# Kernel tuning notes

Hardware: AMD Instinct MI355X
Metric: run time of the kernel (lower is better)

The kernel has to match this reference:

```python
import jax, jax.numpy as jnp
import numpy as np

N = 50000      # nodes
E = 800000     # random edges (self-loops added in reference, per PyG GATConv default)
F_IN = 128
B = 512        # graphs in the batch
NEG_SLOPE = 0.2  # PyG GATConv leaky_relu default


def setup_inputs() -> dict:
    key = jax.random.key(0)
    ks = jax.random.split(key, 12)
    def w(k, shape, fan_in):
        return jax.random.normal(k, shape, jnp.float32) / np.sqrt(fan_in)
    return {
        "x": jax.random.normal(ks[0], (N, F_IN), jnp.float32),
        "edge_index": jax.random.randint(ks[1], (2, E), 0, N, dtype=jnp.int32),
        "batch": jnp.sort(jax.random.randint(ks[2], (N,), 0, B, dtype=jnp.int32)),
        "W1": w(ks[3], (F_IN, 4 * 64), F_IN),
        "a_src1": w(ks[4], (4, 64), 64),
        "a_dst1": w(ks[5], (4, 64), 64),
        "b1": jnp.zeros((4 * 64,), jnp.float32),
        "W2": w(ks[6], (256, 1 * 128), 256),
        "a_src2": w(ks[7], (1, 128), 128),
        "a_dst2": w(ks[8], (1, 128), 128),
        "b2": jnp.zeros((128,), jnp.float32),
        "Wl": w(ks[9], (128, 1), 128),
        "bl": jnp.zeros((1,), jnp.float32),
    }


def gat_layer(x, src, dst, W, a_src, a_dst, b, n):
    H, Fo = a_src.shape
    h = (x @ W).reshape(n, H, Fo)                      # [N,H,Fo]
    alpha_s = jnp.einsum("nhf,hf->nh", h, a_src)       # [N,H]
    alpha_d = jnp.einsum("nhf,hf->nh", h, a_dst)
    e = jax.nn.leaky_relu(alpha_s[src] + alpha_d[dst], NEG_SLOPE)  # [E,H]
    # segment softmax over incoming edges of each dst node
    m = jax.ops.segment_max(e, dst, num_segments=n)    # [N,H]; self-loops => every node hit
    ex = jnp.exp(e - m[dst])
    den = jax.ops.segment_sum(ex, dst, num_segments=n)
    alpha = ex / den[dst]                              # [E,H]
    out = jax.ops.segment_sum(h[src] * alpha[:, :, None], dst, num_segments=n)
    return out.reshape(n, H * Fo) + b


def reference(x, edge_index, batch, W1, a_src1, a_dst1, b1, W2, a_src2, a_dst2, b2, Wl, bl):
    n = x.shape[0]
    loops = jnp.arange(n, dtype=edge_index.dtype)
    src = jnp.concatenate([edge_index[0], loops])
    dst = jnp.concatenate([edge_index[1], loops])
    h = jax.nn.elu(gat_layer(x, src, dst, W1, a_src1, a_dst1, b1, n))
    h = jax.nn.elu(gat_layer(h, src, dst, W2, a_src2, a_dst2, b2, n))
    # dropout omitted (inference)
    sums = jax.ops.segment_sum(h, batch, num_segments=B)
    cnt = jax.ops.segment_sum(jnp.ones((n,), h.dtype), batch, num_segments=B)
    g = sums / jnp.maximum(cnt, 1.0)[:, None]          # global_mean_pool -> [B,128]
    return jax.nn.sigmoid(g @ Wl + bl).reshape(-1)     # [B]
```

## Files before the change

kernel.cpp:

```cpp
#include <hip/hip_runtime.h>
#include <hip/hip_bf16.h>

#define NN 50000
#define EE 800000
#define ETOT 850000
#define BB 512
#define CAP 64
#define NPART 8
#define DPP 6250

typedef __hip_bfloat16 bf16;
typedef __attribute__((ext_vector_type(8))) __bf16 v8bf;
typedef __attribute__((ext_vector_type(4))) float f32x4;

__device__ __forceinline__ float lo2f(unsigned int u) {
    return __uint_as_float(u << 16);
}
__device__ __forceinline__ float hi2f(unsigned int u) {
    return __uint_as_float(u & 0xffff0000u);
}
__device__ __forceinline__ float us2f(unsigned short u) {
    return __uint_as_float(((unsigned int)u) << 16);
}
__device__ __forceinline__ unsigned short f2bfbits(float f) {
    bf16 h = __float2bfloat16(f);
    return *reinterpret_cast<unsigned short*>(&h);
}
__device__ __forceinline__ float lrelu_exp(float ev) {
    ev = ev > 0.f ? ev : 0.2f * ev;
    return __expf(fminf(ev, 80.f));
}

__global__ void k_prep(const float* __restrict__ W1, const float* __restrict__ W2,
                       bf16* __restrict__ wt1, bf16* __restrict__ wt2,
                       int* __restrict__ deg) {
    int idx = blockIdx.x * blockDim.x + threadIdx.x;
    if (idx < 256 * 128) {
        int c = idx >> 7, k = idx & 127;
        wt1[idx] = __float2bfloat16(W1[k * 256 + c]);
    } else {
        int j = idx - 256 * 128;
        int c = j >> 8, k = j & 255;
        wt2[j] = __float2bfloat16(W2[k * 128 + c]);
    }
    if (idx < NN) deg[idx] = 0;
}

__global__ void k_scatter(const int* __restrict__ srcArr, const int* __restrict__ dstArr,
                          int* __restrict__ deg, int* __restrict__ csrc) {
    int part = blockIdx.x & (NPART - 1);
    int e = (blockIdx.x >> 3) * 256 + threadIdx.x;
    if (e >= ETOT) return;
    int d, s;
    if (e < EE) { d = dstArr[e]; s = srcArr[e]; }
    else        { d = e - EE;    s = d; }
    d = min(max(d, 0), NN - 1);
    s = min(max(s, 0), NN - 1);
    int lo = part * DPP;
    if (d >= lo && d < lo + DPP) {
        int p = atomicAdd(&deg[d], 1);
        if (p < CAP) csrc[d * CAP + p] = s;
    }
}

__global__ __launch_bounds__(256, 2)
void k_gemm1(const float* __restrict__ x, const bf16* __restrict__ wt1,
             const float* __restrict__ aw_s, const float* __restrict__ aw_d,
             bf16* __restrict__ h1, float* __restrict__ as1,
             float* __restrict__ ad1) {
    int n0 = blockIdx.x * 32;
    int t = threadIdx.x;
    __shared__ bf16 xs[32 * 136];
    for (int i = 0; i < 4; i++) {
        int idx = t + 256 * i;
        int r = idx >> 5, c4 = idx & 31;
        float4 v = make_float4(0.f, 0.f, 0.f, 0.f);
        if (n0 + r < NN) v = *(const float4*)(x + (size_t)(n0 + r) * 128 + c4 * 4);
        ushort4 o;
        o.x = f2bfbits(v.x); o.y = f2bfbits(v.y);
        o.z = f2bfbits(v.z); o.w = f2bfbits(v.w);
        *(ushort4*)(&xs[r * 136 + c4 * 4]) = o;
    }
    __syncthreads();

    int wv = t >> 6, lane = t & 63;
    int q = lane >> 4, r16 = lane & 15;
    int rowBase = (wv & 1) * 16;
    int colBase = (wv >> 1) * 128;

    f32x4 acc[8];
#pragma unroll
    for (int ct = 0; ct < 8; ct++) acc[ct] = (f32x4){0.f, 0.f, 0.f, 0.f};

#pragma unroll
    for (int kt = 0; kt < 4; kt++) {
        v8bf va = *(const v8bf*)(&xs[(rowBase + r16) * 136 + kt * 32 + q * 8]);
#pragma unroll
        for (int ct = 0; ct < 8; ct++) {
            v8bf vb = *(const v8bf*)(wt1 + (size_t)(colBase + ct * 16 + r16) * 128 + kt * 32 + q * 8);
            acc[ct] = __builtin_amdgcn_mfma_f32_16x16x32_bf16(va, vb, acc[ct], 0, 0, 0);
        }
    }

    float wsv[8], wdv[8];
#pragma unroll
    for (int ct = 0; ct < 8; ct++) {
        int col = colBase + ct * 16 + r16;
        wsv[ct] = aw_s[col];
        wdv[ct] = aw_d[col];
    }

    float ps[4][2], pd[4][2];
#pragma unroll
    for (int reg = 0; reg < 4; reg++) {
        ps[reg][0] = 0.f; ps[reg][1] = 0.f;
        pd[reg][0] = 0.f; pd[reg][1] = 0.f;
    }

#pragma unroll
    for (int reg = 0; reg < 4; reg++) {
        int node = n0 + rowBase + q * 4 + reg;
        bool ok = node < NN;
#pragma unroll
        for (int ct = 0; ct < 8; ct++) {
            float v = acc[ct][reg];
            if (ok) h1[(size_t)node * 256 + colBase + ct * 16 + r16] = __float2bfloat16(v);
            ps[reg][ct >> 2] += v * wsv[ct];
            pd[reg][ct >> 2] += v * wdv[ct];
        }
    }

#pragma unroll
    for (int reg = 0; reg < 4; reg++) {
        int node = n0 + rowBase + q * 4 + reg;
        bool ok = node < NN;
#pragma unroll
        for (int lh = 0; lh < 2; lh++) {
            float a = ps[reg][lh], b = pd[reg][lh];
            for (int mask = 1; mask <= 8; mask <<= 1) {
                a += __shfl_xor(a, mask);
                b += __shfl_xor(b, mask);
            }
            if (r16 == 0 && ok) {
                int head = (wv >> 1) * 2 + lh;
                as1[node * 4 + head] = a;
                ad1[node * 4 + head] = b;
            }
        }
    }
}

__global__ __launch_bounds__(128, 8)
void k_gather1(const int* __restrict__ csrc, const int* __restrict__ deg,
               const bf16* __restrict__ h1, const float* __restrict__ as1,
               const float* __restrict__ ad1, const float* __restrict__ b1,
               bf16* __restrict__ x2) {
    int n = blockIdx.x;
    int t = threadIdx.x;
    int slice = t >> 6;
    int u = t & 63;
    int lhG = slice * 2 + (u >> 5);
    int cnt = min(deg[n], CAP);
    __shared__ unsigned int ls[CAP];
    __shared__ float la[4 * CAP];
    const char* h1c = (const char*)h1;
    unsigned int tconst = (unsigned int)(slice * 128 + u * 2) * 2;
    if (t < cnt) {
        int s = csrc[n * CAP + t];
        s = min(max(s, 0), NN - 1);
        ls[t] = (unsigned int)s << 9;
        float4 as = *(const float4*)&as1[s * 4];
        float4 ad = *(const float4*)&ad1[n * 4];
        la[0 * CAP + t] = lrelu_exp(as.x + ad.x);
        la[1 * CAP + t] = lrelu_exp(as.y + ad.y);
        la[2 * CAP + t] = lrelu_exp(as.z + ad.z);
        la[3 * CAP + t] = lrelu_exp(as.w + ad.w);
    }
    __syncthreads();
    const float* lah = &la[lhG * CAP];
    float a0 = 0.f, a1 = 0.f, ssum = 0.f;
    int j = 0;
    for (; j + 3 < cnt; j += 4) {
        uint4 ov = *(const uint4*)&ls[j];
        float4 Av = *(const float4*)&lah[j];
        unsigned int o0 = ov.x + tconst, o1 = ov.y + tconst;
        unsigned int o2 = ov.z + tconst, o3 = ov.w + tconst;
        unsigned int u0 = *(const unsigned int*)(h1c + o0);
        unsigned int u1 = *(const unsigned int*)(h1c + o1);
        unsigned int u2 = *(const unsigned int*)(h1c + o2);
        unsigned int u3 = *(const unsigned int*)(h1c + o3);
        ssum += (Av.x + Av.y) + (Av.z + Av.w);
        a0 = fmaf(Av.x, lo2f(u0), a0); a0 = fmaf(Av.y, lo2f(u1), a0);
        a0 = fmaf(Av.z, lo2f(u2), a0); a0 = fmaf(Av.w, lo2f(u3), a0);
        a1 = fmaf(Av.x, hi2f(u0), a1); a1 = fmaf(Av.y, hi2f(u1), a1);
        a1 = fmaf(Av.z, hi2f(u2), a1); a1 = fmaf(Av.w, hi2f(u3), a1);
    }
    for (; j < cnt; j++) {
        unsigned int o0 = ls[j] + tconst;
        float A0 = lah[j];
        unsigned int u0 = *(const unsigned int*)(h1c + o0);
        ssum += A0;
        a0 = fmaf(A0, lo2f(u0), a0);
        a1 = fmaf(A0, hi2f(u0), a1);
    }
    float inv = 1.f / fmaxf(ssum, 1e-35f);
    int c = slice * 128 + u * 2;
    float r0 = a0 * inv + b1[c + 0];
    float r1 = a1 * inv + b1[c + 1];
    r0 = r0 > 0.f ? r0 : (__expf(r0) - 1.f);
    r1 = r1 > 0.f ? r1 : (__expf(r1) - 1.f);
    unsigned int packed = (unsigned int)f2bfbits(r0) | ((unsigned int)f2bfbits(r1) << 16);
    *(unsigned int*)((unsigned short*)x2 + (size_t)n * 256 + c) = packed;
}

__global__ __launch_bounds__(256, 2)
void k_gemm2(const bf16* __restrict__ x2, const bf16* __restrict__ wt2,
             const float* __restrict__ aw_s, const float* __restrict__ aw_d,
             bf16* __restrict__ h2, float* __restrict__ as2,
             float* __restrict__ ad2) {
    int n0 = blockIdx.x * 32;
    int t = threadIdx.x;
    __shared__ bf16 xs[32 * 264];
    __shared__ float psPart[32][2];
    __shared__ float pdPart[32][2];
    for (int i = 0; i < 4; i++) {
        int idx = t + 256 * i;
        int r = idx >> 5, c8 = idx & 31;
        uint4 v;
        if (n0 + r < NN) v = *(const uint4*)(x2 + (size_t)(n0 + r) * 256 + c8 * 8);
        else             v = make_uint4(0, 0, 0, 0);
        *(uint4*)(&xs[r * 264 + c8 * 8]) = v;
    }
    __syncthreads();

    int wv = t >> 6, lane = t & 63;
    int q = lane >> 4, r16 = lane & 15;
    int rowBase = (wv & 1) * 16;
    int colBase = (wv >> 1) * 64;

    f32x4 acc[4];
#pragma unroll
    for (int ct = 0; ct < 4; ct++) acc[ct] = (f32x4){0.f, 0.f, 0.f, 0.f};

#pragma unroll
    for (int kt = 0; kt < 8; kt++) {
        v8bf va = *(const v8bf*)(&xs[(rowBase + r16) * 264 + kt * 32 + q * 8]);
#pragma unroll
        for (int ct = 0; ct < 4; ct++) {
            v8bf vb = *(const v8bf*)(wt2 + (size_t)(colBase + ct * 16 + r16) * 256 + kt * 32 + q * 8);
            acc[ct] = __builtin_amdgcn_mfma_f32_16x16x32_bf16(va, vb, acc[ct], 0, 0, 0);
        }
    }

    float wsv[4], wdv[4];
#pragma unroll
    for (int ct = 0; ct < 4; ct++) {
        int col = colBase + ct * 16 + r16;
        wsv[ct] = aw_s[col];
        wdv[ct] = aw_d[col];
    }

#pragma unroll
    for (int reg = 0; reg < 4; reg++) {
        int node = n0 + rowBase + q * 4 + reg;
        bool ok = node < NN;
        float ps = 0.f, pd = 0.f;
#pragma unroll
        for (int ct = 0; ct < 4; ct++) {
            float v = acc[ct][reg];
            if (ok) h2[(size_t)node * 128 + colBase + ct * 16 + r16] = __float2bfloat16(v);
            ps += v * wsv[ct];
            pd += v * wdv[ct];
        }
        for (int mask = 1; mask <= 8; mask <<= 1) {
            ps += __shfl_xor(ps, mask);
            pd += __shfl_xor(pd, mask);
        }
        if (r16 == 0) {
            int li = rowBase + q * 4 + reg;
            psPart[li][wv >> 1] = ps;
            pdPart[li][wv >> 1] = pd;
        }
    }
    __syncthreads();
    if (t < 32) {
        int node = n0 + t;
        if (node < NN) {
            as2[node] = psPart[t][0] + psPart[t][1];
            ad2[node] = pdPart[t][0] + pdPart[t][1];
        }
    }
}

__global__ __launch_bounds__(128, 8)
void k_gather2(const int* __restrict__ csrc, const int* __restrict__ deg,
               const bf16* __restrict__ h2, const float* __restrict__ as2,
               const float* __restrict__ ad2, const float* __restrict__ b2,
               bf16* __restrict__ hf) {
    int wv = threadIdx.x >> 6;
    int n = blockIdx.x * 2 + wv;
    int t = threadIdx.x & 63;
    int cnt = min(deg[n], CAP);
    float adn = ad2[n];
    __shared__ unsigned int ls[2][CAP];
    __shared__ float la[2][CAP];
    const char* h2c = (const char*)h2;
    unsigned int tconst = (unsigned int)t * 4;
    if (t < cnt) {
        int s = csrc[n * CAP + t];
        s = min(max(s, 0), NN - 1);
        ls[wv][t] = (unsigned int)s << 8;
        la[wv][t] = lrelu_exp(as2[s] + adn);
    }
    __syncthreads();
    float a0 = 0.f, a1 = 0.f, ssum = 0.f;
    int j = 0;
    for (; j + 3 < cnt; j += 4) {
        uint4 ov = *(const uint4*)&ls[wv][j];
        float4 Av = *(const float4*)&la[wv][j];
        unsigned int o0 = ov.x + tconst, o1 = ov.y + tconst;
        unsigned int o2 = ov.z + tconst, o3 = ov.w + tconst;
        unsigned int u0 = *(const unsigned int*)(h2c + o0);
        unsigned int u1 = *(const unsigned int*)(h2c + o1);
        unsigned int u2 = *(const unsigned int*)(h2c + o2);
        unsigned int u3 = *(const unsigned int*)(h2c + o3);
        ssum += (Av.x + Av.y) + (Av.z + Av.w);
        a0 = fmaf(Av.x, lo2f(u0), a0); a0 = fmaf(Av.y, lo2f(u1), a0);
        a0 = fmaf(Av.z, lo2f(u2), a0); a0 = fmaf(Av.w, lo2f(u3), a0);
        a1 = fmaf(Av.x, hi2f(u0), a1); a1 = fmaf(Av.y, hi2f(u1), a1);
        a1 = fmaf(Av.z, hi2f(u2), a1); a1 = fmaf(Av.w, hi2f(u3), a1);
    }
    for (; j < cnt; j++) {
        unsigned int o0 = ls[wv][j] + tconst;
        float A0 = la[wv][j];
        unsigned int u0 = *(const unsigned int*)(h2c + o0);
        ssum += A0;
        a0 = fmaf(A0, lo2f(u0), a0);
        a1 = fmaf(A0, hi2f(u0), a1);
    }
    float inv = 1.f / fmaxf(ssum, 1e-35f);
    int c = t * 2;
    float r0 = a0 * inv + b2[c + 0];
    float r1 = a1 * inv + b2[c + 1];
    r0 = r0 > 0.f ? r0 : (__expf(r0) - 1.f);
    r1 = r1 > 0.f ? r1 : (__expf(r1) - 1.f);
    unsigned int packed = (unsigned int)f2bfbits(r0) | ((unsigned int)f2bfbits(r1) << 16);
    *(unsigned int*)((unsigned short*)hf + (size_t)n * 128 + c) = packed;
}

__global__ void k_pool(const bf16* __restrict__ hf, const int* __restrict__ batch,
                       const float* __restrict__ Wl, const float* __restrict__ bl,
                       float* __restrict__ out) {
    int b = blockIdx.x;
    int t = threadIdx.x;
    int lo = 0, hi = NN;
    while (lo < hi) { int m = (lo + hi) >> 1; if (batch[m] < b) lo = m + 1; else hi = m; }
    int start = lo;
    int lo2 = start, hi2 = NN;
    while (lo2 < hi2) { int m = (lo2 + hi2) >> 1; if (batch[m] < b + 1) lo2 = m + 1; else hi2 = m; }
    int end = lo2;
    const unsigned short* hu = (const unsigned short*)hf;
    float sum = 0.f;
    for (int n = start; n < end; n++) sum += us2f(hu[(size_t)n * 128 + t]);
    int c = end - start;
    float g = sum / (float)(c > 0 ? c : 1);
    float p = g * Wl[t];
    for (int o = 32; o > 0; o >>= 1) p += __shfl_down(p, o);
    __shared__ float red[2];
    if ((t & 63) == 0) red[t >> 6] = p;
    __syncthreads();
    if (t == 0) {
        float acc = red[0] + red[1] + bl[0];
        out[b] = 1.f / (1.f + __expf(-acc));
    }
}

extern "C" void kernel_launch(void* const* d_in, const int* in_sizes, int n_in,
                              void* d_out, int out_size, void* d_ws, size_t ws_size,
                              hipStream_t stream) {
    const float* x = (const float*)d_in[0];
    const int* ei = (const int*)d_in[1];
    const int* batch = (const int*)d_in[2];
    const float* W1 = (const float*)d_in[3];
    const float* aw_s1 = (const float*)d_in[4];
    const float* aw_d1 = (const float*)d_in[5];
    const float* b1 = (const float*)d_in[6];
    const float* W2 = (const float*)d_in[7];
    const float* aw_s2 = (const float*)d_in[8];
    const float* aw_d2 = (const float*)d_in[9];
    const float* b2 = (const float*)d_in[10];
    const float* Wl = (const float*)d_in[11];
    const float* bl = (const float*)d_in[12];
    const int* srcArr = ei;
    const int* dstArr = ei + EE;

    char* w = (char*)d_ws;
    size_t off = 0;
    auto alloc = [&](size_t bytes) -> void* {
        void* p = (void*)(w + off);
        off = (off + bytes + 255) & ~(size_t)255;
        return p;
    };
    bf16* bufA = (bf16*)alloc((size_t)NN * 256 * 2);
    bf16* bufB = (bf16*)alloc((size_t)NN * 256 * 2);
    int* csrc = (int*)alloc((size_t)NN * CAP * 4);
    float* as1 = (float*)alloc((size_t)NN * 4 * 4);
    float* ad1 = (float*)alloc((size_t)NN * 4 * 4);
    float* as2 = (float*)alloc((size_t)NN * 4);
    float* ad2 = (float*)alloc((size_t)NN * 4);
    int* deg = (int*)alloc((size_t)NN * 4);
    bf16* wt1 = (bf16*)alloc((size_t)256 * 128 * 2);
    bf16* wt2 = (bf16*)alloc((size_t)128 * 256 * 2);
    (void)ws_size;

    k_prep<<<256, 256, 0, stream>>>(W1, W2, wt1, wt2, deg);
    int chunks = (ETOT + 255) / 256;
    k_scatter<<<chunks * NPART, 256, 0, stream>>>(srcArr, dstArr, deg, csrc);

    bf16* h1 = bufA;
    bf16* x2 = bufB;
    k_gemm1<<<(NN + 31) / 32, 256, 0, stream>>>(x, wt1, aw_s1, aw_d1, h1, as1, ad1);
    k_gather1<<<NN, 128, 0, stream>>>(csrc, deg, h1, as1, ad1, b1, x2);

    bf16* h2 = bufA;
    k_gemm2<<<(NN + 31) / 32, 256, 0, stream>>>(x2, wt2, aw_s2, aw_d2, h2, as2, ad2);

    bf16* hf = bufB;
    k_gather2<<<NN / 2, 128, 0, stream>>>(csrc, deg, h2, as2, ad2, b2, hf);

    k_pool<<<BB, 128, 0, stream>>>(hf, batch, Wl, bl, (float*)d_out);
}
```

Measured before the change: 336.7 us.

## Remap GAT gathers to one wave per node with wider loads and deeper unroll

```diff
diff --git a/kernel.cpp b/kernel.cpp
--- a/kernel.cpp
+++ b/kernel.cpp
@@ -150,67 +150,106 @@
     }
 }
 
-__global__ __launch_bounds__(128, 8)
+__global__ __launch_bounds__(256, 6)
 void k_gather1(const int* __restrict__ csrc, const int* __restrict__ deg,
                const bf16* __restrict__ h1, const float* __restrict__ as1,
                const float* __restrict__ ad1, const float* __restrict__ b1,
                bf16* __restrict__ x2) {
-    int n = blockIdx.x;
-    int t = threadIdx.x;
-    int slice = t >> 6;
-    int u = t & 63;
-    int lhG = slice * 2 + (u >> 5);
+    int wv = threadIdx.x >> 6;
+    int n = blockIdx.x * 4 + wv;
+    int l = threadIdx.x & 63;
     int cnt = min(deg[n], CAP);
-    __shared__ unsigned int ls[CAP];
-    __shared__ float la[4 * CAP];
-    const char* h1c = (const char*)h1;
-    unsigned int tconst = (unsigned int)(slice * 128 + u * 2) * 2;
-    if (t < cnt) {
-        int s = csrc[n * CAP + t];
+    __shared__ unsigned int ls[4][CAP];
+    __shared__ float la[4][4 * 68];
+    if (l < cnt) {
+        int s = csrc[n * CAP + l];
         s = min(max(s, 0), NN - 1);
-        ls[t] = (unsigned int)s << 9;
+        ls[wv][l] = (unsigned int)s << 9;
         float4 as = *(const float4*)&as1[s * 4];
         float4 ad = *(const float4*)&ad1[n * 4];
-        la[0 * CAP + t] = lrelu_exp(as.x + ad.x);
-        la[1 * CAP + t] = lrelu_exp(as.y + ad.y);
-        la[2 * CAP + t] = lrelu_exp(as.z + ad.z);
-        la[3 * CAP + t] = lrelu_exp(as.w + ad.w);
-    }
-    __syncthreads();
-    const float* lah = &la[lhG * CAP];
-    float a0 = 0.f, a1 = 0.f, ssum = 0.f;
+        la[wv][0 * 68 + l] = lrelu_exp(as.x + ad.x);
+        la[wv][1 * 68 + l] = lrelu_exp(as.y + ad.y);
+        la[wv][2 * 68 + l] = lrelu_exp(as.z + ad.z);
+        la[wv][3 * 68 + l] = lrelu_exp(as.w + ad.w);
+    }
+    __syncthreads();
+    const unsigned int* lsw = ls[wv];
+    const float* lah = &la[wv][(l >> 4) * 68];
+    const char* h1c = (const char*)h1;
+    unsigned int tconst = (unsigned int)l * 8;
+    float a0 = 0.f, a1 = 0.f, a2 = 0.f, a3 = 0.f, ssum = 0.f;
     int j = 0;
+    for (; j + 7 < cnt; j += 8) {
+        uint4 ov0 = *(const uint4*)&lsw[j];
+        uint4 ov1 = *(const uint4*)&lsw[j + 4];
+        float4 A0 = *(const float4*)&lah[j];
+        float4 A1 = *(const float4*)&lah[j + 4];
+        uint2 d0 = *(const uint2*)(h1c + (ov0.x + tconst));
+        uint2 d1 = *(const uint2*)(h1c + (ov0.y + tconst));
+        uint2 d2 = *(const uint2*)(h1c + (ov0.z + tconst));
+        uint2 d3 = *(const uint2*)(h1c + (ov0.w + tconst));
+        uint2 d4 = *(const uint2*)(h1c + (ov1.x + tconst));
+        uint2 d5 = *(const uint2*)(h1c + (ov1.y + tconst));
+        uint2 d6 = *(const uint2*)(h1c + (ov1.z + tconst));
+        uint2 d7 = *(const uint2*)(h1c + (ov1.w + tconst));
+        ssum += (A0.x + A0.y) + (A0.z + A0.w) + (A1.x + A1.y) + (A1.z + A1.w);
+        a0 = fmaf(A0.x, lo2f(d0.x), a0); a1 = fmaf(A0.x, hi2f(d0.x), a1);
+        a2 = fmaf(A0.x, lo2f(d0.y), a2); a3 = fmaf(A0.x, hi2f(d0.y), a3);
+        a0 = fmaf(A0.y, lo2f(d1.x), a0); a1 = fmaf(A0.y, hi2f(d1.x), a1);
+        a2 = fmaf(A0.y, lo2f(d1.y), a2); a3 = fmaf(A0.y, hi2f(d1.y), a3);
+        a0 = fmaf(A0.z, lo2f(d2.x), a0); a1 = fmaf(A0.z, hi2f(d2.x), a1);
+        a2 = fmaf(A0.z, lo2f(d2.y), a2); a3 = fmaf(A0.z, hi2f(d2.y), a3);
+        a0 = fmaf(A0.w, lo2f(d3.x), a0); a1 = fmaf(A0.w, hi2f(d3.x), a1);
+        a2 = fmaf(A0.w, lo2f(d3.y), a2); a3 = fmaf(A0.w, hi2f(d3.y), a3);
+        a0 = fmaf(A1.x, lo2f(d4.x), a0); a1 = fmaf(A1.x, hi2f(d4.x), a1);
+        a2 = fmaf(A1.x, lo2f(d4.y), a2); a3 = fmaf(A1.x, hi2f(d4.y), a3);
+        a0 = fmaf(A1.y, lo2f(d5.x), a0); a1 = fmaf(A1.y, hi2f(d5.x), a1);
+        a2 = fmaf(A1.y, lo2f(d5.y), a2); a3 = fmaf(A1.y, hi2f(d5.y), a3);
+        a0 = fmaf(A1.z, lo2f(d6.x), a0); a1 = fmaf(A1.z, hi2f(d6.x), a1);
+        a2 = fmaf(A1.z, lo2f(d6.y), a2); a3 = fmaf(A1.z, hi2f(d6.y), a3);
+        a0 = fmaf(A1.w, lo2f(d7.x), a0); a1 = fmaf(A1.w, hi2f(d7.x), a1);
+        a2 = fmaf(A1.w, lo2f(d7.y), a2); a3 = fmaf(A1.w, hi2f(d7.y), a3);
+    }
     for (; j + 3 < cnt; j += 4) {
-        uint4 ov = *(const uint4*)&ls[j];
-        float4 Av = *(const float4*)&lah[j];
-        unsigned int o0 = ov.x + tconst, o1 = ov.y + tconst;
-        unsigned int o2 = ov.z + tconst, o3 = ov.w + tconst;
-        unsigned int u0 = *(const unsigned int*)(h1c + o0);
-        unsigned int u1 = *(const unsigned int*)(h1c + o1);
-        unsigned int u2 = *(const unsigned int*)(h1c + o2);
-        unsigned int u3 = *(const unsigned int*)(h1c + o3);
-        ssum += (Av.x + Av.y) + (Av.z + Av.w);
-        a0 = fmaf(Av.x, lo2f(u0), a0); a0 = fmaf(Av.y, lo2f(u1), a0);
-        a0 = fmaf(Av.z, lo2f(u2), a0); a0 = fmaf(Av.w, lo2f(u3), a0);
-        a1 = fmaf(Av.x, hi2f(u0), a1); a1 = fmaf(Av.y, hi2f(u1), a1);
-        a1 = fmaf(Av.z, hi2f(u2), a1); a1 = fmaf(Av.w, hi2f(u3), a1);
+        uint4 ov0 = *(const uint4*)&lsw[j];
+        float4 A0 = *(const float4*)&lah[j];
+        uint2 d0 = *(const uint2*)(h1c + (ov0.x + tconst));
+        uint2 d1 = *(const uint2*)(h1c + (ov0.y + tconst));
+        uint2 d2 = *(const uint2*)(h1c + (ov0.z + tconst));
+        uint2 d3 = *(const uint2*)(h1c + (ov0.w + tconst));
+        ssum += (A0.x + A0.y) + (A0.z + A0.w);
+        a0 = fmaf(A0.x, lo2f(d0.x), a0); a1 = fmaf(A0.x, hi2f(d0.x), a1);
+        a2 = fmaf(A0.x, lo2f(d0.y), a2); a3 = fmaf(A0.x, hi2f(d0.y), a3);
+        a0 = fmaf(A0.y, lo2f(d1.x), a0); a1 = fmaf(A0.y, hi2f(d1.x), a1);
+        a2 = fmaf(A0.y, lo2f(d1.y), a2); a3 = fmaf(A0.y, hi2f(d1.y), a3);
+        a0 = fmaf(A0.z, lo2f(d2.x), a0); a1 = fmaf(A0.z, hi2f(d2.x), a1);
+        a2 = fmaf(A0.z, lo2f(d2.y), a2); a3 = fmaf(A0.z, hi2f(d2.y), a3);
+        a0 = fmaf(A0.w, lo2f(d3.x), a0); a1 = fmaf(A0.w, hi2f(d3.x), a1);
+        a2 = fmaf(A0.w, lo2f(d3.y), a2); a3 = fmaf(A0.w, hi2f(d3.y), a3);
     }
     for (; j < cnt; j++) {
-        unsigned int o0 = ls[j] + tconst;
+        unsigned int o0 = lsw[j] + tconst;
         float A0 = lah[j];
-        unsigned int u0 = *(const unsigned int*)(h1c + o0);
+        uint2 d0 = *(const uint2*)(h1c + o0);
         ssum += A0;
-        a0 = fmaf(A0, lo2f(u0), a0);
-        a1 = fmaf(A0, hi2f(u0), a1);
+        a0 = fmaf(A0, lo2f(d0.x), a0); a1 = fmaf(A0, hi2f(d0.x), a1);
+        a2 = fmaf(A0, lo2f(d0.y), a2); a3 = fmaf(A0, hi2f(d0.y), a3);
     }
     float inv = 1.f / fmaxf(ssum, 1e-35f);
-    int c = slice * 128 + u * 2;
-    float r0 = a0 * inv + b1[c + 0];
-    float r1 = a1 * inv + b1[c + 1];
+    int c = l * 4;
+    float4 bv = *(const float4*)&b1[c];
+    float r0 = a0 * inv + bv.x;
+    float r1 = a1 * inv + bv.y;
+    float r2 = a2 * inv + bv.z;
+    float r3 = a3 * inv + bv.w;
     r0 = r0 > 0.f ? r0 : (__expf(r0) - 1.f);
     r1 = r1 > 0.f ? r1 : (__expf(r1) - 1.f);
-    unsigned int packed = (unsigned int)f2bfbits(r0) | ((unsigned int)f2bfbits(r1) << 16);
-    *(unsigned int*)((unsigned short*)x2 + (size_t)n * 256 + c) = packed;
+    r2 = r2 > 0.f ? r2 : (__expf(r2) - 1.f);
+    r3 = r3 > 0.f ? r3 : (__expf(r3) - 1.f);
+    uint2 packed;
+    packed.x = (unsigned int)f2bfbits(r0) | ((unsigned int)f2bfbits(r1) << 16);
+    packed.y = (unsigned int)f2bfbits(r2) | ((unsigned int)f2bfbits(r3) << 16);
+    *(uint2*)((unsigned short*)x2 + (size_t)n * 256 + c) = packed;
 }
 
 __global__ __launch_bounds__(256, 2)
@@ -292,47 +331,69 @@
     }
 }
 
-__global__ __launch_bounds__(128, 8)
+__global__ __launch_bounds__(256, 6)
 void k_gather2(const int* __restrict__ csrc, const int* __restrict__ deg,
                const bf16* __restrict__ h2, const float* __restrict__ as2,
                const float* __restrict__ ad2, const float* __restrict__ b2,
                bf16* __restrict__ hf) {
     int wv = threadIdx.x >> 6;
-    int n = blockIdx.x * 2 + wv;
+    int n = blockIdx.x * 4 + wv;
     int t = threadIdx.x & 63;
     int cnt = min(deg[n], CAP);
-    float adn = ad2[n];
-    __shared__ unsigned int ls[2][CAP];
-    __shared__ float la[2][CAP];
+    __shared__ unsigned int ls[4][CAP];
+    __shared__ float la[4][CAP];
     const char* h2c = (const char*)h2;
     unsigned int tconst = (unsigned int)t * 4;
     if (t < cnt) {
         int s = csrc[n * CAP + t];
         s = min(max(s, 0), NN - 1);
         ls[wv][t] = (unsigned int)s << 8;
-        la[wv][t] = lrelu_exp(as2[s] + adn);
-    }
-    __syncthreads();
+        la[wv][t] = lrelu_exp(as2[s] + ad2[n]);
+    }
+    __syncthreads();
+    const unsigned int* lsw = ls[wv];
+    const float* law = la[wv];
     float a0 = 0.f, a1 = 0.f, ssum = 0.f;
     int j = 0;
+    for (; j + 7 < cnt; j += 8) {
+        uint4 ov0 = *(const uint4*)&lsw[j];
+        uint4 ov1 = *(const uint4*)&lsw[j + 4];
+        float4 A0 = *(const float4*)&law[j];
+        float4 A1 = *(const float4*)&law[j + 4];
+        unsigned int u0 = *(const unsigned int*)(h2c + (ov0.x + tconst));
+        unsigned int u1 = *(const unsigned int*)(h2c + (ov0.y + tconst));
+        unsigned int u2 = *(const unsigned int*)(h2c + (ov0.z + tconst));
+        unsigned int u3 = *(const unsigned int*)(h2c + (ov0.w + tconst));
+        unsigned int u4 = *(const unsigned int*)(h2c + (ov1.x + tconst));
+        unsigned int u5 = *(const unsigned int*)(h2c + (ov1.y + tconst));
+        unsigned int u6 = *(const unsigned int*)(h2c + (ov1.z + tconst));
+        unsigned int u7 = *(const unsigned int*)(h2c + (ov1.w + tconst));
+        ssum += (A0.x + A0.y) + (A0.z + A0.w) + (A1.x + A1.y) + (A1.z + A1.w);
+        a0 = fmaf(A0.x, lo2f(u0), a0); a1 = fmaf(A0.x, hi2f(u0), a1);
+        a0 = fmaf(A0.y, lo2f(u1), a0); a1 = fmaf(A0.y, hi2f(u1), a1);
+        a0 = fmaf(A0.z, lo2f(u2), a0); a1 = fmaf(A0.z, hi2f(u2), a1);
+        a0 = fmaf(A0.w, lo2f(u3), a0); a1 = fmaf(A0.w, hi2f(u3), a1);
+        a0 = fmaf(A1.x, lo2f(u4), a0); a1 = fmaf(A1.x, hi2f(u4), a1);
+        a0 = fmaf(A1.y, lo2f(u5), a0); a1 = fmaf(A1.y, hi2f(u5), a1);
+        a0 = fmaf(A1.z, lo2f(u6), a0); a1 = fmaf(A1.z, hi2f(u6), a1);
+        a0 = fmaf(A1.w, lo2f(u7), a0); a1 = fmaf(A1.w, hi2f(u7), a1);
+    }
     for (; j + 3 < cnt; j += 4) {
-        uint4 ov = *(const uint4*)&ls[wv][j];
-        float4 Av = *(const float4*)&la[wv][j];
-        unsigned int o0 = ov.x + tconst, o1 = ov.y + tconst;
-        unsigned int o2 = ov.z + tconst, o3 = ov.w + tconst;
-        unsigned int u0 = *(const unsigned int*)(h2c + o0);
-        unsigned int u1 = *(const unsigned int*)(h2c + o1);
-        unsigned int u2 = *(const unsigned int*)(h2c + o2);
-        unsigned int u3 = *(const unsigned int*)(h2c + o3);
-        ssum += (Av.x + Av.y) + (Av.z + Av.w);
-        a0 = fmaf(Av.x, lo2f(u0), a0); a0 = fmaf(Av.y, lo2f(u1), a0);
-        a0 = fmaf(Av.z, lo2f(u2), a0); a0 = fmaf(Av.w, lo2f(u3), a0);
-        a1 = fmaf(Av.x, hi2f(u0), a1); a1 = fmaf(Av.y, hi2f(u1), a1);
-        a1 = fmaf(Av.z, hi2f(u2), a1); a1 = fmaf(Av.w, hi2f(u3), a1);
+        uint4 ov0 = *(const uint4*)&lsw[j];
+        float4 A0 = *(const float4*)&law[j];
+        unsigned int u0 = *(const unsigned int*)(h2c + (ov0.x + tconst));
+        unsigned int u1 = *(const unsigned int*)(h2c + (ov0.y + tconst));
+        unsigned int u2 = *(const unsigned int*)(h2c + (ov0.z + tconst));
+        unsigned int u3 = *(const unsigned int*)(h2c + (ov0.w + tconst));
+        ssum += (A0.x + A0.y) + (A0.z + A0.w);
+        a0 = fmaf(A0.x, lo2f(u0), a0); a1 = fmaf(A0.x, hi2f(u0), a1);
+        a0 = fmaf(A0.y, lo2f(u1), a0); a1 = fmaf(A0.y, hi2f(u1), a1);
+        a0 = fmaf(A0.z, lo2f(u2), a0); a1 = fmaf(A0.z, hi2f(u2), a1);
+        a0 = fmaf(A0.w, lo2f(u3), a0); a1 = fmaf(A0.w, hi2f(u3), a1);
     }
     for (; j < cnt; j++) {
-        unsigned int o0 = ls[wv][j] + tconst;
-        float A0 = la[wv][j];
+        unsigned int o0 = lsw[j] + tconst;
+        float A0 = law[j];
         unsigned int u0 = *(const unsigned int*)(h2c + o0);
         ssum += A0;
         a0 = fmaf(A0, lo2f(u0), a0);
@@ -420,13 +481,13 @@
     bf16* h1 = bufA;
     bf16* x2 = bufB;
     k_gemm1<<<(NN + 31) / 32, 256, 0, stream>>>(x, wt1, aw_s1, aw_d1, h1, as1, ad1);
-    k_gather1<<<NN, 128, 0, stream>>>(csrc, deg, h1, as1, ad1, b1, x2);
+    k_gather1<<<NN / 4, 256, 0, stream>>>(csrc, deg, h1, as1, ad1, b1, x2);
 
     bf16* h2 = bufA;
     k_gemm2<<<(NN + 31) / 32, 256, 0, stream>>>(x2, wt2, aw_s2, aw_d2, h2, as2, ad2);
 
     bf16* hf = bufB;
-    k_gather2<<<NN / 2, 128, 0, stream>>>(csrc, deg, h2, as2, ad2, b2, hf);
+    k_gather2<<<NN / 4, 256, 0, stream>>>(csrc, deg, h2, as2, ad2, b2, hf);
 
     k_pool<<<BB, 128, 0, stream>>>(hf, batch, Wl, bl, (float*)d_out);
 }
```

After: 335.0 us. Within noise of the previous version (-0.5%).
